# Performance work log

Hardware: AMD Instinct MI355X
Metric: run time of the kernel (lower is better)

## Reference

```python
import jax, jax.numpy as jnp
import numpy as np

N_HASHES = 4
CHUNK = 144


def conv2d(x, w, b, pad):
    y = jax.lax.conv_general_dilated(x, w, (1, 1), [(pad, pad), (pad, pad)],
                                     dimension_numbers=('NCHW', 'OIHW', 'NCHW'))
    return y + b[None, :, None, None]


def resblock(x, w1, b1, w2, b2, ws=None, bs=None):
    # conv3x3 -> ReLU -> conv3x3 + skip (1x1 projection when channels change)
    h = conv2d(x, w1, b1, 1)
    h = jax.nn.relu(h)
    h = conv2d(h, w2, b2, 1)
    skip = x if ws is None else conv2d(x, ws, bs, 0)
    return skip + h


def _forward(feature_dec1, feature_dec2, reference_feature,
             mw1, mb1, mw2, mb2, mws, mbs,
             a1w1, a1b1, a1w2, a1b2, a2w1, a2b1, a2w2, a2b2,
             random_index):
    fd1 = jax.lax.stop_gradient(feature_dec1)  # is_detach=True default
    fd2 = jax.lax.stop_gradient(feature_dec2)
    B, C0, H, W = fd1.shape
    L = H * W
    # embeddings: (B, L, C) with C = C0 // reduction, and (B, L, C0) assemblies
    f1 = resblock(fd1, mw1, mb1, mw2, mb2, mws, mbs).reshape(B, -1, L).transpose(0, 2, 1)
    f2 = resblock(fd2, mw1, mb1, mw2, mb2, mws, mbs).reshape(B, -1, L).transpose(0, 2, 1)
    aux1 = resblock(fd1, a1w1, a1b1, a1w2, a1b2).reshape(B, -1, L).transpose(0, 2, 1)
    refe = resblock(reference_feature, a2w1, a2b1, a2w2, a2b2).reshape(B, -1, L).transpose(0, 2, 1)
    C = f1.shape[-1]
    inv_random_index = jnp.argsort(random_index)
    hb = min(2 * L // CHUNK + (2 * L // CHUNK) % 2, 128)
    f1f2 = jnp.concatenate([f1, f2], axis=1)            # (B, 2L, C)
    # LSH hashing (random rotations drawn with a fixed key, matching randn-per-call in torch)
    rot = jax.random.normal(jax.random.key(42), (C, N_HASHES, hb // 2), dtype=f1f2.dtype)
    rv = jnp.einsum('btf,fhi->bhti', f1f2, rot)
    rv = jnp.concatenate([rv, -rv], axis=-1)
    codes = jnp.argmax(rv, axis=-1)                     # (B, nh, 2L)
    codes = codes + (jnp.arange(N_HASHES) * hb)[None, :, None]
    codes = codes[:, :, random_index].reshape(B, -1)    # (B, nh*2L)
    indices = jnp.argsort(codes, axis=-1)
    undo_sort = jnp.argsort(indices, axis=-1)
    mod_indices = (indices % 2) * L                     # faithful to torch `indices % 2 * L` precedence
    zo = jnp.concatenate([jnp.full((B, L), 0.01, f1.dtype),
                          jnp.full((B, L), 0.99, f1.dtype)], axis=1)
    f1f2_p = f1f2[:, random_index, :]
    q = jnp.take_along_axis(f1f2_p, mod_indices[:, :, None], axis=1)
    zo_p = zo[:, random_index]
    z = jnp.take_along_axis(zo_p, mod_indices, axis=1)
    refw = jnp.concatenate([aux1, refe], axis=1)[:, random_index, :]
    r = jnp.take_along_axis(refw, mod_indices[:, :, None], axis=1)
    rem = (2 * L) % CHUNK
    padding = CHUNK - rem if rem != 0 else 0
    qb = q.reshape(B, N_HASHES, 2 * L, C)
    zb = z.reshape(B, N_HASHES, 2 * L)
    rb = r.reshape(B, N_HASHES, 2 * L, -1)
    if padding:
        qb = jnp.concatenate([qb, qb[:, :, -padding:]], axis=2)
        zb = jnp.concatenate([zb, zb[:, :, -padding:]], axis=2)
        rb = jnp.concatenate([rb, rb[:, :, -padding:]], axis=2)
    k = qb.shape[2] // CHUNK
    qb = qb.reshape(B, N_HASHES, k, CHUNK, C)
    zb = zb.reshape(B, N_HASHES, k, CHUNK)
    rb = rb.reshape(B, N_HASHES, k, CHUNK, -1)
    # F.normalize(p=2, dim=-1, eps=5e-5)
    norm = jnp.sqrt(jnp.sum(qb * qb, axis=-1, keepdims=True))
    km = qb / jnp.maximum(norm, 5e-5)
    adj = lambda x: jnp.concatenate([x, jnp.roll(x, 1, axis=2), jnp.roll(x, -1, axis=2)], axis=3)
    km, zb3, rb3 = adj(km), adj(zb), adj(rb)            # keys/vals over 3 adjacent buckets
    raw = jnp.einsum('bhkie,bhkje->bhkij', qb, km)      # (B,nh,k,144,432)
    w = jnp.exp(raw) * zb3[:, :, :, None, :]
    denom = jnp.sum(w, axis=-1, keepdims=True)
    score = w / denom
    bucket_score = denom.reshape(B, N_HASHES, -1)
    ret = jnp.einsum('bhkij,bhkje->bhkie', score, rb3)  # (B,nh,k,144,C0)
    CR = rb3.shape[-1]
    ret = ret.reshape(B, N_HASHES, -1, CR)
    if padding:
        ret = ret[:, :, :-padding]
        bucket_score = bucket_score[:, :, :-padding]
    ret = ret.reshape(B, N_HASHES * 2 * L, CR)
    bucket_score = bucket_score.reshape(B, -1)
    ret = jnp.take_along_axis(ret, undo_sort[:, :, None], axis=1)
    bucket_score = jnp.take_along_axis(bucket_score, undo_sort, axis=1)
    ret = ret.reshape(B, N_HASHES, 2 * L, CR)
    bucket_score = bucket_score.reshape(B, N_HASHES, 2 * L, 1)
    probs = bucket_score / jnp.sum(bucket_score, axis=1, keepdims=True)
    ret = jnp.sum(ret * probs, axis=1)                  # (B, 2L, CR)
    ret = ret.transpose(0, 2, 1)[:, :, inv_random_index]
    return ret.reshape(B, CR, 2, H, W)[:, :, 0]         # (B, C0, H, W)


def setup_inputs() -> dict:
    key = jax.random.key(0)
    ks = jax.random.split(key, 12)
    B, C0, H, W = 2, 64, 100, 100
    red = 4
    Cm = C0 // red
    s = jnp.float32(0.05)
    rn = lambda i, shape: jax.random.normal(ks[i], shape, dtype=jnp.float32)
    return {
        'feature_dec1': rn(0, (B, C0, H, W)),
        'feature_dec2': rn(1, (B, C0, H, W)),
        'reference_feature': rn(2, (B, C0, H, W)),
        'random_index': jax.random.permutation(ks[3], 2 * H * W).astype(jnp.int32),
        'mw1': rn(4, (Cm, C0, 3, 3)) * s, 'mb1': jnp.zeros((Cm,), jnp.float32),
        'mw2': rn(5, (Cm, Cm, 3, 3)) * s, 'mb2': jnp.zeros((Cm,), jnp.float32),
        'mws': rn(6, (Cm, C0, 1, 1)) * s, 'mbs': jnp.zeros((Cm,), jnp.float32),
        'a1w1': rn(7, (C0, C0, 3, 3)) * s, 'a1b1': jnp.zeros((C0,), jnp.float32),
        'a1w2': rn(8, (C0, C0, 3, 3)) * s, 'a1b2': jnp.zeros((C0,), jnp.float32),
        'a2w1': rn(9, (C0, C0, 3, 3)) * s, 'a2b1': jnp.zeros((C0,), jnp.float32),
        'a2w2': rn(10, (C0, C0, 3, 3)) * s, 'a2b2': jnp.zeros((C0,), jnp.float32),
    }


def reference(feature_dec1, feature_dec2, reference_feature, random_index,
              mw1, mb1, mw2, mb2, mws, mbs,
              a1w1, a1b1, a1w2, a1b2, a2w1, a2b1, a2w2, a2b2):
    return _forward(feature_dec1, feature_dec2, reference_feature,
                    mw1, mb1, mw2, mb2, mws, mbs,
                    a1w1, a1b1, a1w2, a1b2, a2w1, a2b1, a2w2, a2b2,
                    random_index)
```

## Files before the change

### kernel.cpp

```cpp
#include <hip/hip_runtime.h>

#define JAX_THREEFRY_PARTITIONABLE 1

namespace {

constexpr int BN   = 2;
constexpr int C0   = 64;
constexpr int HH   = 100;
constexpr int WWW  = 100;
constexpr int LL   = 10000;
constexpr int TL   = 20000;
constexpr int CHK  = 144;
constexpr int NCHK = 139;
constexpr int NPAD = 16;
constexpr int WINR = 432;

constexpr int OFF_HT0  = 0;
constexpr int OFF_HT1  = OFF_HT0 + 640000;
constexpr int OFF_HT2  = OFF_HT1 + 640000;
constexpr int OFF_HT3  = OFF_HT2 + 640000;
constexpr int OFF_F    = OFF_HT3 + 640000;
constexpr int OFF_SC   = OFF_F + 640000;
constexpr int OFF_CODE = OFF_SC + 272;
constexpr int OFF_RANK = OFF_CODE + 40000;
constexpr int OFF_N0   = OFF_RANK + 160000;
constexpr int OFF_INV  = OFF_N0 + 1112;

__device__ __forceinline__ unsigned rotl32(unsigned v, int r) {
  return (v << r) | (v >> (32 - r));
}

__device__ void tf2x32(unsigned k0, unsigned k1, unsigned x0, unsigned x1,
                       unsigned& o0, unsigned& o1) {
  unsigned ks2 = k0 ^ k1 ^ 0x1BD11BDAu;
  x0 += k0; x1 += k1;
#define TFR(r) { x0 += x1; x1 = rotl32(x1, r); x1 ^= x0; }
  TFR(13) TFR(15) TFR(26) TFR(6)  x0 += k1;  x1 += ks2 + 1u;
  TFR(17) TFR(29) TFR(16) TFR(24) x0 += ks2; x1 += k0 + 2u;
  TFR(13) TFR(15) TFR(26) TFR(6)  x0 += k0;  x1 += k1 + 3u;
  TFR(17) TFR(29) TFR(16) TFR(24) x0 += k1;  x1 += ks2 + 4u;
  TFR(13) TFR(15) TFR(26) TFR(6)  x0 += ks2; x1 += k0 + 5u;
#undef TFR
  o0 = x0; o1 = x1;
}

__device__ float xla_erfinv(float x) {
#pragma clang fp contract(off)
  float w = -log1pf(-x * x);
  float p;
  if (w < 5.0f) {
    w = w - 2.5f;
    p = 2.81022636e-08f;
    p = 3.43273939e-07f  + p * w;
    p = -3.5233877e-06f  + p * w;
    p = -4.39150654e-06f + p * w;
    p = 0.00021858087f   + p * w;
    p = -0.00125372503f  + p * w;
    p = -0.00417768164f  + p * w;
    p = 0.246640727f     + p * w;
    p = 1.50140941f      + p * w;
  } else {
    w = sqrtf(w) - 3.0f;
    p = -0.000200214257f;
    p = 0.000100950558f + p * w;
    p = 0.00134934322f  + p * w;
    p = -0.00367342844f + p * w;
    p = 0.00573950773f  + p * w;
    p = -0.0076224613f  + p * w;
    p = 0.00943887047f  + p * w;
    p = 1.00167406f     + p * w;
    p = 2.83297682f     + p * w;
  }
  return p * x;
}

__device__ float rot_rng(int i) {
  unsigned o0, o1, bits;
#if JAX_THREEFRY_PARTITIONABLE
  tf2x32(0u, 42u, 0u, (unsigned)i, o0, o1);
  bits = o0 ^ o1;
#else
  if (i < 2048) { tf2x32(0u, 42u, (unsigned)i, (unsigned)(i + 2048), o0, o1); bits = o0; }
  else          { tf2x32(0u, 42u, (unsigned)(i - 2048), (unsigned)i, o0, o1); bits = o1; }
#endif
  unsigned fb = (bits >> 9) | 0x3f800000u;
  float f = __uint_as_float(fb) - 1.0f;
  const float lo = __uint_as_float(0xBF7FFFFFu);
  float u = fmaxf(lo, f * 2.0f + lo);
  return __uint_as_float(0x3FB504F3u) * xla_erfinv(u);
}

__global__ __launch_bounds__(512) void k_conv1(
    const float* __restrict__ fd1, const float* __restrict__ fd2,
    const float* __restrict__ mw1,
    float* __restrict__ ht0, float* __restrict__ ht1,
    float* __restrict__ ht2, float* __restrict__ ht3) {
  int x = blockIdx.x;
  int blk = (x & 7) * 182 + (x >> 3);
  int kq = blk & 3;
  int rest = blk >> 2;
  int n = rest / 91, tile = rest % 91;
  int yt = tile / 7, xt = tile % 7;
  int ty0 = yt * 8, tx0 = xt * 16;
  const float* in = ((n >> 1) ? fd2 : fd1) + (n & 1) * (C0 * LL) + (kq * 16) * LL;
  float* htk = ((kq == 0) ? ht0 : (kq == 1) ? ht1 : (kq == 2) ? ht2 : ht3) + n * 16 * LL;
  int tid = threadIdx.x;
  int co = tid & 15, xq = (tid >> 4) & 3, yl = tid >> 6;

  __shared__ float sIn[16 * 10 * 20];
  __shared__ float sW[144 * 16];

  for (int i = tid; i < 144 * 16; i += 512) {
    int o = i & 15, r = i >> 4;
    sW[i] = mw1[o * 576 + kq * 144 + r];
  }
  for (int idx = tid; idx < 16 * 10 * 18; idx += 512) {
    int ci = idx / 180, r = idx % 180, iy = r / 18, ix = r % 18;
    int gy = ty0 - 1 + iy, gx = tx0 - 1 + ix;
    float v = 0.f;
    if (gy >= 0 && gy < HH && gx >= 0 && gx < WWW) v = in[ci * LL + gy * WWW + gx];
    sIn[ci * 200 + iy * 20 + ix] = v;
  }
  __syncthreads();

  float acc[4];
#pragma unroll
  for (int p = 0; p < 4; ++p) acc[p] = 0.f;

  for (int cc = 0; cc < 4; ++cc) {
    float w[4][9];
#pragma unroll
    for (int c4 = 0; c4 < 4; ++c4)
#pragma unroll
      for (int t = 0; t < 9; ++t)
        w[c4][t] = sW[((cc * 4 + c4) * 9 + t) * 16 + co];
#pragma unroll
    for (int c4 = 0; c4 < 4; ++c4) {
      const float* rowb = &sIn[(cc * 4 + c4) * 200 + yl * 20 + xq * 4];
#pragma unroll
      for (int dy = 0; dy < 3; ++dy) {
        const float* r = rowb + dy * 20;
        float v[6];
#pragma unroll
        for (int k = 0; k < 6; ++k) v[k] = r[k];
#pragma unroll
        for (int dx = 0; dx < 3; ++dx) {
          float wv = w[c4][dy * 3 + dx];
#pragma unroll
          for (int p = 0; p < 4; ++p) acc[p] = fmaf(v[p + dx], wv, acc[p]);
        }
      }
    }
  }

  int yv = ty0 + yl;
  int xg = tx0 + xq * 4;
  if (yv < HH && xg < WWW) {
    float4 s = make_float4(acc[0], acc[1], acc[2], acc[3]);
    *(float4*)&htk[co * LL + yv * WWW + xg] = s;
  }
}

__global__ __launch_bounds__(512) void k_conv2(
    const float* __restrict__ fd1, const float* __restrict__ fd2,
    const float* __restrict__ ht0, const float* __restrict__ ht1,
    const float* __restrict__ ht2, const float* __restrict__ ht3,
    const float* __restrict__ mw2, const float* __restrict__ mb1,
    const float* __restrict__ mb2, const float* __restrict__ mws,
    const float* __restrict__ mbs, float* __restrict__ F) {
  int xx = blockIdx.x;
  int xcd = xx & 7, slot = xx >> 3;
  int blk = (xcd < 4) ? (xcd * 46 + slot) : (184 + (xcd - 4) * 45 + slot);
  int n = blk / 91, tile = blk % 91;
  int yt = tile / 7, xt = tile % 7;
  int ty0 = yt * 8, tx0 = xt * 16;
  int src = n >> 1, b = n & 1;
  const float* in = (src ? fd2 : fd1) + b * (C0 * LL);
  const float* h0 = ht0 + n * 16 * LL;
  const float* h1 = ht1 + n * 16 * LL;
  const float* h2 = ht2 + n * 16 * LL;
  const float* h3 = ht3 + n * 16 * LL;
  int tid = threadIdx.x;
  int co = tid & 15, xq = (tid >> 4) & 3, yl = tid >> 6;

  __shared__ float sW2[144 * 16];
  __shared__ float sWs[64 * 16];
  __shared__ float sH[16 * 10 * 20];
  __shared__ float sSkip[16 * 8 * 17];

  for (int i = tid; i < 144 * 16; i += 512) {
    int o = i & 15, r = i >> 4;
    sW2[i] = mw2[o * 144 + r];
  }
  for (int i = tid; i < 64 * 16; i += 512) {
    int o = i & 15, ci = i >> 4;
    sWs[i] = mws[o * 64 + ci];
  }
  for (int idx = tid; idx < 16 * 10 * 18; idx += 512) {
    int ci = idx / 180, r = idx % 180, iy = r / 18, ix = r % 18;
    int gy = ty0 - 1 + iy, gx = tx0 - 1 + ix;
    float v = 0.f;
    if (gy >= 0 && gy < HH && gx >= 0 && gx < WWW) {
      int o = ci * LL + gy * WWW + gx;
      v = fmaxf(h0[o] + h1[o] + h2[o] + h3[o] + mb1[ci], 0.f);
    }
    sH[ci * 200 + iy * 20 + ix] = v;
  }
  __syncthreads();

  float acc[4];
  float bias = mb2[co] + mbs[co];
#pragma unroll
  for (int p = 0; p < 4; ++p) acc[p] = bias;

  for (int ci = 0; ci < 16; ++ci) {
    const float* rowb = &sH[ci * 200 + yl * 20 + xq * 4];
#pragma unroll
    for (int dy = 0; dy < 3; ++dy) {
      const float* r = rowb + dy * 20;
      float v[6];
#pragma unroll
      for (int k = 0; k < 6; ++k) v[k] = r[k];
#pragma unroll
      for (int dx = 0; dx < 3; ++dx) {
        float wv = sW2[(ci * 9 + dy * 3 + dx) * 16 + co];
#pragma unroll
        for (int p = 0; p < 4; ++p) acc[p] = fmaf(v[p + dx], wv, acc[p]);
      }
    }
  }

  for (int cc = 0; cc < 4; ++cc) {
    __syncthreads();
    for (int idx = tid; idx < 16 * 8 * 16; idx += 512) {
      int ci = idx >> 7, r = idx & 127, iy = r >> 4, ix = r & 15;
      int gy = ty0 + iy, gx = tx0 + ix;
      float v = 0.f;
      if (gy < HH && gx < WWW) v = in[(cc * 16 + ci) * LL + gy * WWW + gx];
      sSkip[(ci * 8 + iy) * 17 + ix] = v;
    }
    __syncthreads();
    for (int c16 = 0; c16 < 16; ++c16) {
      float wv = sWs[(cc * 16 + c16) * 16 + co];
      const float* sv = &sSkip[(c16 * 8 + yl) * 17 + xq * 4];
#pragma unroll
      for (int p = 0; p < 4; ++p) acc[p] = fmaf(sv[p], wv, acc[p]);
    }
  }

  int yv = ty0 + yl;
  if (yv < HH) {
    float* Fb = F + (b * TL + src * LL + yv * WWW) * 16 + co;
#pragma unroll
    for (int p = 0; p < 4; ++p) {
      int xv = tx0 + xq * 4 + p;
      if (xv < WWW) Fb[xv * 16] = acc[p];
    }
  }
}

__global__ __launch_bounds__(576) void k_codes(
    const float* __restrict__ F, const int* __restrict__ ri,
    unsigned char* __restrict__ codes,
    const float* __restrict__ fd1, const float* __restrict__ refin,
    const float* __restrict__ a1w1, const float* __restrict__ a1b1,
    const float* __restrict__ a1w2, const float* __restrict__ a1b2,
    const float* __restrict__ a2w1, const float* __restrict__ a2b1,
    const float* __restrict__ a2w2, const float* __restrict__ a2b2,
    float* __restrict__ SC, int* __restrict__ inv) {
  int blk = blockIdx.x;
  int tid = threadIdx.x;

  if (blk < 280) {
    int bh = blk / 35, seg = blk % 35;
    int b = bh >> 2, h = bh & 3;
    __shared__ float srot[1024];
    for (int l = tid; l < 1024; l += 576) {
      int j = l >> 4, c = l & 15;
      srot[l] = rot_rng(c * 256 + h * 64 + j);
    }
    __syncthreads();
    int t = seg * 576 + tid;
    if (t >= TL) return;
    int pos = ri[t];
    const float* Fr = F + (b * TL + pos) * 16;
    float q[16];
#pragma unroll
    for (int c = 0; c < 16; ++c) q[c] = Fr[c];
    float best = -1e30f; int bi = 0;
    float worst = 1e30f; int wi = 0;
    for (int j = 0; j < 64; ++j) {
      float v = 0.f;
      const float* rp = srot + j * 16;
#pragma unroll
      for (int c = 0; c < 16; ++c) v = fmaf(q[c], rp[c], v);
      if (v > best)  { best = v;  bi = j; }
      if (v < worst) { worst = v; wi = j; }
    }
    int code = (best >= -worst) ? bi : (64 + wi);
    codes[bh * TL + t] = (unsigned char)code;
    return;
  }

  if (blk >= 285) {
    int t = (blk - 285) * 576 + tid;
    if (t < TL) {
      int p = ri[t];
      if (p < LL) inv[p] = t;
    }
    return;
  }

  if (blk == 284) {
#pragma clang fp contract(off)
    int b = tid;
    if (b >= BN) return;
    int j0 = ri[0], jL = ri[LL];
    const float* qA = F + (b * TL + j0) * 16;
    const float* qB = F + (b * TL + jL) * 16;
    float nA = 0.f, nB = 0.f;
    for (int c = 0; c < 16; ++c) { nA += qA[c] * qA[c]; nB += qB[c] * qB[c]; }
    float mA = fmaxf(sqrtf(nA), 5e-5f), mB = fmaxf(sqrtf(nB), 5e-5f);
    float d00 = 0.f, d01 = 0.f, d10 = 0.f, d11 = 0.f;
    for (int c = 0; c < 16; ++c) {
      float kAc = qA[c] / mA, kBc = qB[c] / mB;
      d00 += qA[c] * kAc; d01 += qA[c] * kBc;
      d10 += qB[c] * kAc; d11 += qB[c] * kBc;
    }
    float zA = (j0 < LL) ? 0.01f : 0.99f;
    float zB = (jL < LL) ? 0.01f : 0.99f;
    float* sc = SC + b * 136;
    sc[0] = expf(d00) * zA; sc[1] = expf(d01) * zB;
    sc[2] = expf(d10) * zA; sc[3] = expf(d11) * zB;
    return;
  }

  int pb = blk - 280;
  int b = pb & 1, which = pb >> 1;
  int pos = ri[which * LL];
  const float *in, *w1, *b1, *w2, *b2;
  int sp;
  if (pos < LL) {
    in = fd1 + b * C0 * LL; w1 = a1w1; b1 = a1b1; w2 = a1w2; b2 = a1b2; sp = pos;
  } else {
    in = refin + b * C0 * LL; w1 = a2w1; b1 = a2b1; w2 = a2w2; b2 = a2b2;
    sp = pos - LL;
  }
  int y = sp / WWW, x = sp % WWW;

  __shared__ float sPatch[64][25];
  __shared__ float sW[144 * 64];
  __shared__ float sH[9][64];
  __shared__ float sPart[9][64];

  for (int idx = tid; idx < 64 * 25; idx += 576) {
    int ci = idx / 25, pp = idx % 25;
    int gy = y - 2 + pp / 5, gx = x - 2 + pp % 5;
    float v = 0.f;
    if (gy >= 0 && gy < HH && gx >= 0 && gx < WWW) v = in[ci * LL + gy * WWW + gx];
    sPatch[ci][pp] = v;
  }

  int p = tid / 64, ch = tid & 63;
  int p3 = p / 3, pm = p % 3;
  int yy = y + p3 - 1, xx = x + pm - 1;
  bool inb = (yy >= 0) && (yy < HH) && (xx >= 0) && (xx < WWW);

  float acc0 = 0.f, acc1 = 0.f;
  for (int cc = 0; cc < 4; ++cc) {
    __syncthreads();
    for (int i = tid; i < 144 * 64; i += 576) {
      int chh = i & 63, rl = i >> 6;
      sW[i] = w1[chh * 576 + cc * 144 + rl];
    }
    __syncthreads();
    if (inb) {
#pragma unroll
      for (int ci = 0; ci < 16; ++ci) {
        const float* wp = &sW[ci * 9 * 64 + ch];
        const float* pr = &sPatch[cc * 16 + ci][0];
#pragma unroll
        for (int t = 0; t < 9; ++t) {
          float v = pr[(p3 + t / 3) * 5 + (pm + t % 3)];
          if (ci & 1) acc1 = fmaf(v, wp[t * 64], acc1);
          else        acc0 = fmaf(v, wp[t * 64], acc0);
        }
      }
    }
  }
  sH[p][ch] = inb ? fmaxf(acc0 + acc1 + b1[ch], 0.f) : 0.f;
  __syncthreads();

  {
    float part = 0.f;
    for (int ci = 0; ci < 64; ++ci)
      part = fmaf(sH[p][ci], w2[ch * 576 + ci * 9 + p], part);
    sPart[p][ch] = part;
  }
  __syncthreads();
  if (tid < 64) {
    int co = tid;
    float a = in[co * LL + y * WWW + x] + b2[co];
#pragma unroll
    for (int g = 0; g < 9; ++g) a += sPart[g][co];
    SC[b * 136 + 4 + which * 64 + co] = a;
  }
}

__global__ __launch_bounds__(256) void k_sort(
    const unsigned char* __restrict__ codes,
    int* __restrict__ rank_of, int* __restrict__ n0g) {
  int bh = blockIdx.x;
  const unsigned int* keys4 = (const unsigned int*)(codes + bh * TL);
  __shared__ unsigned short cnt[128 * 241];
  __shared__ unsigned int sup[128 * 16];
  __shared__ unsigned int totalsL[128];
  __shared__ unsigned int baseoff[128];
  __shared__ unsigned int n0s[NCHK];
  __shared__ unsigned int wtot;
  int tid = threadIdx.x;

  for (int i = tid; i < 128 * 241 / 2; i += 256) ((unsigned int*)cnt)[i] = 0u;
  for (int i = tid; i < NCHK; i += 256) n0s[i] = 0u;
  __syncthreads();

  const int SEG = 84;
  int base = tid * SEG;
  int nloc = (tid < 240) ? (TL - base) : 0;
  if (nloc > SEG) nloc = SEG;
  if (nloc < 0) nloc = 0;

  unsigned int kw[21];
  int nw = (nloc + 3) >> 2;
  for (int w = 0; w < nw; ++w) kw[w] = keys4[tid * 21 + w];

  for (int e = 0; e < nloc; ++e) {
    int c = (kw[e >> 2] >> ((e & 3) * 8)) & 255;
    cnt[c * 241 + tid]++;
  }
  __syncthreads();

  for (int idx = tid; idx < 128 * 15; idx += 256) {
    int c = idx / 15, s = idx % 15;
    unsigned int sum = 0;
#pragma unroll
    for (int k = 0; k < 16; ++k) sum += cnt[c * 241 + 16 * s + k];
    sup[c * 16 + s] = sum;
  }
  __syncthreads();

  if (tid < 128) {
    unsigned int run = 0;
#pragma unroll
    for (int s = 0; s < 15; ++s) {
      unsigned int t = sup[tid * 16 + s];
      sup[tid * 16 + s] = run;
      run += t;
    }
    totalsL[tid] = run;
  }
  __syncthreads();

  {
    unsigned int v = 0;
    if (tid < 128) {
      v = totalsL[tid];
#pragma unroll
      for (int d = 1; d < 64; d <<= 1) {
        unsigned int o = __shfl_up(v, d);
        if ((tid & 63) >= d) v += o;
      }
      if (tid == 63) wtot = v;
    }
    __syncthreads();
    if (tid < 128) {
      unsigned int incl = v + ((tid >= 64) ? wtot : 0u);
      baseoff[tid] = incl - totalsL[tid];
    }
  }
  __syncthreads();

  for (int idx = tid; idx < 128 * 15; idx += 256) {
    int c = idx / 15, s = idx % 15;
    unsigned int run = baseoff[c] + sup[c * 16 + s];
#pragma unroll
    for (int k = 0; k < 16; ++k) {
      int g = 16 * s + k;
      unsigned int t = cnt[c * 241 + g];
      cnt[c * 241 + g] = (unsigned short)run;
      run += t;
    }
  }
  __syncthreads();

  for (int e = 0; e < nloc; ++e) {
    int idx = base + e;
    int c = (kw[e >> 2] >> ((e & 3) * 8)) & 255;
    unsigned int r = cnt[c * 241 + tid]++;
    rank_of[bh * TL + idx] = (int)r;
    if (!(idx & 1)) {
      atomicAdd(&n0s[r / CHK], 1u);
      if (r >= TL - NPAD) atomicAdd(&n0s[NCHK - 1], 1u);
    }
  }
  __syncthreads();
  for (int i = tid; i < NCHK; i += 256) n0g[bh * NCHK + i] = (int)n0s[i];
}

__global__ __launch_bounds__(256) void k_out(
    const int* __restrict__ inv, const int* __restrict__ rank_of,
    const int* __restrict__ n0, const float* __restrict__ SC,
    float* __restrict__ out) {
  int b = blockIdx.y;
  int c0 = blockIdx.z * 16;
  int p = blockIdx.x * 256 + threadIdx.x;
  if (p >= LL) return;
  int t = inv[p];
  int si = t & 1;
  float e0 = SC[b * 136 + si * 2 + 0];
  float e1 = SC[b * 136 + si * 2 + 1];
  float s0 = 0.f, s1 = 0.f;
  for (int h = 0; h < 4; ++h) {
    int r = rank_of[(b * 4 + h) * TL + t];
    int k = r / CHK;
    int km = (k == 0) ? NCHK - 1 : k - 1;
    int kp = (k == NCHK - 1) ? 0 : k + 1;
    const int* nb = n0 + (b * 4 + h) * NCHK;
    int W0 = nb[k] + nb[km] + nb[kp];
    s0 += (float)W0 * e0;
    s1 += (float)(WINR - W0) * e1;
  }
  float invd = 1.f / (s0 + s1);
  float al = s0 * invd;
  float be = s1 * invd;
  const float* rA = SC + b * 136 + 4;
  const float* rB = rA + 64;
  float* o = out + b * C0 * LL + p;
#pragma unroll
  for (int c = 0; c < 16; ++c) o[(c0 + c) * LL] = al * rA[c0 + c] + be * rB[c0 + c];
}

}

extern "C" void kernel_launch(void* const* d_in, const int* in_sizes, int n_in,
                              void* d_out, int out_size, void* d_ws, size_t ws_size,
                              hipStream_t stream) {
  const float* fd1  = (const float*)d_in[0];
  const float* fd2  = (const float*)d_in[1];
  const float* reff = (const float*)d_in[2];
  const int*   ri   = (const int*)d_in[3];
  const float* mw1  = (const float*)d_in[4];
  const float* mb1  = (const float*)d_in[5];
  const float* mw2  = (const float*)d_in[6];
  const float* mb2  = (const float*)d_in[7];
  const float* mws  = (const float*)d_in[8];
  const float* mbs  = (const float*)d_in[9];
  const float* a1w1 = (const float*)d_in[10];
  const float* a1b1 = (const float*)d_in[11];
  const float* a1w2 = (const float*)d_in[12];
  const float* a1b2 = (const float*)d_in[13];
  const float* a2w1 = (const float*)d_in[14];
  const float* a2b1 = (const float*)d_in[15];
  const float* a2w2 = (const float*)d_in[16];
  const float* a2b2 = (const float*)d_in[17];

  float* ws = (float*)d_ws;
  float* ht0  = ws + OFF_HT0;
  float* ht1  = ws + OFF_HT1;
  float* ht2  = ws + OFF_HT2;
  float* ht3  = ws + OFF_HT3;
  float* F    = ws + OFF_F;
  float* SC   = ws + OFF_SC;
  unsigned char* codes = (unsigned char*)(ws + OFF_CODE);
  int* rank_of = (int*)(ws + OFF_RANK);
  int* n0      = (int*)(ws + OFF_N0);
  int* invp    = (int*)(ws + OFF_INV);

  k_conv1<<<dim3(1456), dim3(512), 0, stream>>>(fd1, fd2, mw1, ht0, ht1, ht2, ht3);
  k_conv2<<<dim3(364), dim3(512), 0, stream>>>(fd1, fd2, ht0, ht1, ht2, ht3, mw2,
                                               mb1, mb2, mws, mbs, F);
  k_codes<<<dim3(320), dim3(576), 0, stream>>>(F, ri, codes, fd1, reff,
                                               a1w1, a1b1, a1w2, a1b2,
                                               a2w1, a2b1, a2w2, a2b2, SC, invp);
  k_sort<<<dim3(8), dim3(256), 0, stream>>>(codes, rank_of, n0);
  k_out<<<dim3(40, 2, 4), dim3(256), 0, stream>>>(invp, rank_of, n0, SC, (float*)d_out);
}
```

Measured before the change: 139.4 us.

## Pretranspose aux weights and precompute LSH rotations in conv1 side blocks

Measured after the change: 122.4 us. 12.2% less time.

```diff
diff --git a/kernel.cpp b/kernel.cpp
--- a/kernel.cpp
+++ b/kernel.cpp
@@ -25,6 +25,10 @@
 constexpr int OFF_RANK = OFF_CODE + 40000;
 constexpr int OFF_N0   = OFF_RANK + 160000;
 constexpr int OFF_INV  = OFF_N0 + 1112;
+constexpr int OFF_AUX  = OFF_INV + 10000;
+constexpr int OFF_ROT  = OFF_AUX + 147456;
+
+constexpr int AUXW = 36864;
 
 __device__ __forceinline__ unsigned rotl32(unsigned v, int r) {
   return (v << r) | (v >> (32 - r));
@@ -93,9 +97,29 @@
 __global__ __launch_bounds__(512) void k_conv1(
     const float* __restrict__ fd1, const float* __restrict__ fd2,
     const float* __restrict__ mw1,
+    const float* __restrict__ a1w1, const float* __restrict__ a1w2,
+    const float* __restrict__ a2w1, const float* __restrict__ a2w2,
     float* __restrict__ ht0, float* __restrict__ ht1,
-    float* __restrict__ ht2, float* __restrict__ ht3) {
+    float* __restrict__ ht2, float* __restrict__ ht3,
+    float* __restrict__ auxT, float* __restrict__ rotT) {
   int x = blockIdx.x;
+  int tid = threadIdx.x;
+  if (x >= 1456) {
+    int idx = (x - 1456) * 512 + tid;
+    if (idx < 4 * AUXW) {
+      int wsel = idx / AUXW, j = idx % AUXW;
+      const float* src = (wsel == 0) ? a1w1 : (wsel == 1) ? a1w2
+                       : (wsel == 2) ? a2w1 : a2w2;
+      int co = j / 576, r = j % 576;
+      auxT[wsel * AUXW + r * 64 + co] = src[j];
+    } else {
+      int i = idx - 4 * AUXW;
+      float rv = rot_rng(i);
+      int c = i >> 8, h = (i >> 6) & 3, jj = i & 63;
+      rotT[(h * 64 + jj) * 16 + c] = rv;
+    }
+    return;
+  }
   int blk = (x & 7) * 182 + (x >> 3);
   int kq = blk & 3;
   int rest = blk >> 2;
@@ -104,15 +128,14 @@
   int ty0 = yt * 8, tx0 = xt * 16;
   const float* in = ((n >> 1) ? fd2 : fd1) + (n & 1) * (C0 * LL) + (kq * 16) * LL;
   float* htk = ((kq == 0) ? ht0 : (kq == 1) ? ht1 : (kq == 2) ? ht2 : ht3) + n * 16 * LL;
-  int tid = threadIdx.x;
   int co = tid & 15, xq = (tid >> 4) & 3, yl = tid >> 6;
 
   __shared__ float sIn[16 * 10 * 20];
-  __shared__ float sW[144 * 16];
-
-  for (int i = tid; i < 144 * 16; i += 512) {
-    int o = i & 15, r = i >> 4;
-    sW[i] = mw1[o * 576 + kq * 144 + r];
+  __shared__ float sW[144 * 17];
+
+  for (int i = tid; i < 2304; i += 512) {
+    int o = i / 144, r = i % 144;
+    sW[r * 17 + o] = mw1[o * 576 + kq * 144 + r];
   }
   for (int idx = tid; idx < 16 * 10 * 18; idx += 512) {
     int ci = idx / 180, r = idx % 180, iy = r / 18, ix = r % 18;
@@ -133,7 +156,7 @@
     for (int c4 = 0; c4 < 4; ++c4)
 #pragma unroll
       for (int t = 0; t < 9; ++t)
-        w[c4][t] = sW[((cc * 4 + c4) * 9 + t) * 16 + co];
+        w[c4][t] = sW[((cc * 4 + c4) * 9 + t) * 17 + co];
 #pragma unroll
     for (int c4 = 0; c4 < 4; ++c4) {
       const float* rowb = &sIn[(cc * 4 + c4) * 200 + yl * 20 + xq * 4];
@@ -183,18 +206,18 @@
   int tid = threadIdx.x;
   int co = tid & 15, xq = (tid >> 4) & 3, yl = tid >> 6;
 
-  __shared__ float sW2[144 * 16];
-  __shared__ float sWs[64 * 16];
+  __shared__ float sW2[144 * 17];
+  __shared__ float sWs[64 * 17];
   __shared__ float sH[16 * 10 * 20];
   __shared__ float sSkip[16 * 8 * 17];
 
-  for (int i = tid; i < 144 * 16; i += 512) {
-    int o = i & 15, r = i >> 4;
-    sW2[i] = mw2[o * 144 + r];
-  }
-  for (int i = tid; i < 64 * 16; i += 512) {
-    int o = i & 15, ci = i >> 4;
-    sWs[i] = mws[o * 64 + ci];
+  for (int i = tid; i < 2304; i += 512) {
+    int o = i / 144, r = i % 144;
+    sW2[r * 17 + o] = mw2[o * 144 + r];
+  }
+  for (int i = tid; i < 1024; i += 512) {
+    int o = i / 64, ci = i % 64;
+    sWs[ci * 17 + o] = mws[o * 64 + ci];
   }
   for (int idx = tid; idx < 16 * 10 * 18; idx += 512) {
     int ci = idx / 180, r = idx % 180, iy = r / 18, ix = r % 18;
@@ -223,7 +246,7 @@
       for (int k = 0; k < 6; ++k) v[k] = r[k];
 #pragma unroll
       for (int dx = 0; dx < 3; ++dx) {
-        float wv = sW2[(ci * 9 + dy * 3 + dx) * 16 + co];
+        float wv = sW2[(ci * 9 + dy * 3 + dx) * 17 + co];
 #pragma unroll
         for (int p = 0; p < 4; ++p) acc[p] = fmaf(v[p + dx], wv, acc[p]);
       }
@@ -241,7 +264,7 @@
     }
     __syncthreads();
     for (int c16 = 0; c16 < 16; ++c16) {
-      float wv = sWs[(cc * 16 + c16) * 16 + co];
+      float wv = sWs[(cc * 16 + c16) * 17 + co];
       const float* sv = &sSkip[(c16 * 8 + yl) * 17 + xq * 4];
 #pragma unroll
       for (int p = 0; p < 4; ++p) acc[p] = fmaf(sv[p], wv, acc[p]);
@@ -260,13 +283,12 @@
 }
 
 __global__ __launch_bounds__(576) void k_codes(
-    const float* __restrict__ F, const int* __restrict__ ri,
-    unsigned char* __restrict__ codes,
+    const float* __restrict__ F, const float* __restrict__ rotT,
+    const int* __restrict__ ri, unsigned char* __restrict__ codes,
     const float* __restrict__ fd1, const float* __restrict__ refin,
-    const float* __restrict__ a1w1, const float* __restrict__ a1b1,
-    const float* __restrict__ a1w2, const float* __restrict__ a1b2,
-    const float* __restrict__ a2w1, const float* __restrict__ a2b1,
-    const float* __restrict__ a2w2, const float* __restrict__ a2b2,
+    const float* __restrict__ auxT,
+    const float* __restrict__ a1b1, const float* __restrict__ a1b2,
+    const float* __restrict__ a2b1, const float* __restrict__ a2b2,
     float* __restrict__ SC, int* __restrict__ inv) {
   int blk = blockIdx.x;
   int tid = threadIdx.x;
@@ -274,12 +296,6 @@
   if (blk < 280) {
     int bh = blk / 35, seg = blk % 35;
     int b = bh >> 2, h = bh & 3;
-    __shared__ float srot[1024];
-    for (int l = tid; l < 1024; l += 576) {
-      int j = l >> 4, c = l & 15;
-      srot[l] = rot_rng(c * 256 + h * 64 + j);
-    }
-    __syncthreads();
     int t = seg * 576 + tid;
     if (t >= TL) return;
     int pos = ri[t];
@@ -287,11 +303,12 @@
     float q[16];
 #pragma unroll
     for (int c = 0; c < 16; ++c) q[c] = Fr[c];
+    const float* rotb = rotT + h * 1024;
     float best = -1e30f; int bi = 0;
     float worst = 1e30f; int wi = 0;
     for (int j = 0; j < 64; ++j) {
       float v = 0.f;
-      const float* rp = srot + j * 16;
+      const float* rp = rotb + j * 16;
 #pragma unroll
       for (int c = 0; c < 16; ++c) v = fmaf(q[c], rp[c], v);
       if (v > best)  { best = v;  bi = j; }
@@ -338,13 +355,13 @@
   int pb = blk - 280;
   int b = pb & 1, which = pb >> 1;
   int pos = ri[which * LL];
-  const float *in, *w1, *b1, *w2, *b2;
+  const float *in, *w1T, *b1, *w2T, *b2;
   int sp;
   if (pos < LL) {
-    in = fd1 + b * C0 * LL; w1 = a1w1; b1 = a1b1; w2 = a1w2; b2 = a1b2; sp = pos;
+    in = fd1 + b * C0 * LL; w1T = auxT; b1 = a1b1; w2T = auxT + AUXW; b2 = a1b2; sp = pos;
   } else {
-    in = refin + b * C0 * LL; w1 = a2w1; b1 = a2b1; w2 = a2w2; b2 = a2b2;
-    sp = pos - LL;
+    in = refin + b * C0 * LL; w1T = auxT + 2 * AUXW; b1 = a2b1; w2T = auxT + 3 * AUXW;
+    b2 = a2b2; sp = pos - LL;
   }
   int y = sp / WWW, x = sp % WWW;
 
@@ -369,10 +386,7 @@
   float acc0 = 0.f, acc1 = 0.f;
   for (int cc = 0; cc < 4; ++cc) {
     __syncthreads();
-    for (int i = tid; i < 144 * 64; i += 576) {
-      int chh = i & 63, rl = i >> 6;
-      sW[i] = w1[chh * 576 + cc * 144 + rl];
-    }
+    for (int i = tid; i < 144 * 64; i += 576) sW[i] = w1T[cc * 9216 + i];
     __syncthreads();
     if (inb) {
 #pragma unroll
@@ -393,8 +407,8 @@
 
   {
     float part = 0.f;
-    for (int ci = 0; ci < 64; ++ci)
-      part = fmaf(sH[p][ci], w2[ch * 576 + ci * 9 + p], part);
+    const float* wbase = w2T + p * 64 + ch;
+    for (int ci = 0; ci < 64; ++ci) part = fmaf(sH[p][ci], wbase[ci * 9 * 64], part);
     sPart[p][ch] = part;
   }
   __syncthreads();
@@ -575,13 +589,15 @@
   int* rank_of = (int*)(ws + OFF_RANK);
   int* n0      = (int*)(ws + OFF_N0);
   int* invp    = (int*)(ws + OFF_INV);
-
-  k_conv1<<<dim3(1456), dim3(512), 0, stream>>>(fd1, fd2, mw1, ht0, ht1, ht2, ht3);
+  float* auxT  = ws + OFF_AUX;
+  float* rotT  = ws + OFF_ROT;
+
+  k_conv1<<<dim3(1752), dim3(512), 0, stream>>>(fd1, fd2, mw1, a1w1, a1w2, a2w1,
+                                                a2w2, ht0, ht1, ht2, ht3, auxT, rotT);
   k_conv2<<<dim3(364), dim3(512), 0, stream>>>(fd1, fd2, ht0, ht1, ht2, ht3, mw2,
                                                mb1, mb2, mws, mbs, F);
-  k_codes<<<dim3(320), dim3(576), 0, stream>>>(F, ri, codes, fd1, reff,
-                                               a1w1, a1b1, a1w2, a1b2,
-                                               a2w1, a2b1, a2w2, a2b2, SC, invp);
+  k_codes<<<dim3(320), dim3(576), 0, stream>>>(F, rotT, ri, codes, fd1, reff, auxT,
+                                               a1b1, a1b2, a2b1, a2b2, SC, invp);
   k_sort<<<dim3(8), dim3(256), 0, stream>>>(codes, rank_of, n0);
   k_out<<<dim3(40, 2, 4), dim3(256), 0, stream>>>(invp, rank_of, n0, SC, (float*)d_out);
 }
```
